# Optimization experiments

Measured on AMD Instinct MI355X. Metric: run time of the kernel, lower is better.

Reference implementation:

```python
import jax, jax.numpy as jnp
import numpy as np

B, S, D = 4, 2048, 1024
H = 16
HD = D // H
PF = 4096
EPS = 1e-5


def setup_inputs() -> dict:
    key = jax.random.key(0)
    ks = jax.random.split(key, 16)
    s = 1.0 / np.sqrt(D)
    inp = {
        'src': jax.random.normal(ks[0], (B, S, D), jnp.float32),
        'Wq': jax.random.normal(ks[1], (D, D), jnp.float32) * s,
        'bq': jnp.zeros((D,), jnp.float32),
        'Wk': jax.random.normal(ks[2], (D, D), jnp.float32) * s,
        'bk': jnp.zeros((D,), jnp.float32),
        'Wv': jax.random.normal(ks[3], (D, D), jnp.float32) * s,
        'bv': jnp.zeros((D,), jnp.float32),
        'Wo': jax.random.normal(ks[4], (D, D), jnp.float32) * s,
        'bo': jnp.zeros((D,), jnp.float32),
        'g1': jnp.ones((D,), jnp.float32),
        'b1': jnp.zeros((D,), jnp.float32),
        'W1': jax.random.normal(ks[5], (D, PF), jnp.float32) * s,
        'bf1': jnp.zeros((PF,), jnp.float32),
        'W2': jax.random.normal(ks[6], (PF, D), jnp.float32) * (1.0 / np.sqrt(PF)),
        'bf2': jnp.zeros((D,), jnp.float32),
        'g2': jnp.ones((D,), jnp.float32),
        'b2': jnp.zeros((D,), jnp.float32),
    }
    return inp


def _layer_norm(x, g, b):
    mu = jnp.mean(x, axis=-1, keepdims=True)
    var = jnp.mean(jnp.square(x - mu), axis=-1, keepdims=True)
    return (x - mu) * jax.lax.rsqrt(var + EPS) * g + b


def reference(src, Wq, bq, Wk, bk, Wv, bv, Wo, bo, g1, b1, W1, bf1, W2, bf2, g2, b2):
    scale = 1.0 / np.sqrt(HD)
    # QKV projections -> [B, H, S, HD]
    q = (src @ Wq + bq).reshape(B, S, H, HD).transpose(0, 2, 1, 3)
    k = (src @ Wk + bk).reshape(B, S, H, HD).transpose(0, 2, 1, 3)
    v = (src @ Wv + bv).reshape(B, S, H, HD).transpose(0, 2, 1, 3)
    # attention scores [B, H, S, S]
    attn = jax.nn.softmax(jnp.einsum('bhqd,bhkd->bhqk', q, k) * scale, axis=-1)
    x = jnp.einsum('bhqk,bhkd->bhqd', attn, v)
    x = x.transpose(0, 2, 1, 3).reshape(B, S, D)
    attn_out = x @ Wo + bo
    # residual + LN (dropout is identity at p=0)
    src1 = _layer_norm(src + attn_out, g1, b1)
    # positionwise FFN: Linear -> Dropout -> ReLU -> Linear
    ff = jax.nn.relu(src1 @ W1 + bf1) @ W2 + bf2
    return _layer_norm(src1 + ff, g2, b2)
```

## Files before the change

kernel.cpp:

```cpp
#include <hip/hip_runtime.h>

#define BB 4
#define SS 2048
#define DD 1024
#define HH 16
#define PFF 4096
#define MR 8192

typedef unsigned short u16;
typedef __attribute__((ext_vector_type(8))) short s16x8;
typedef __attribute__((ext_vector_type(4))) float f32x4v;
typedef __attribute__((ext_vector_type(4))) unsigned short u16x4;
typedef __attribute__((ext_vector_type(8))) unsigned short u16x8;

__device__ inline u16 f2bf(float f) {
  union { float f; unsigned u; } v; v.f = f;
  unsigned r = v.u + 0x7FFFu + ((v.u >> 16) & 1u);
  return (u16)(r >> 16);
}

__device__ inline void gload16(const void* g, void* l) {
  __builtin_amdgcn_global_load_lds(
      (const __attribute__((address_space(1))) void*)g,
      (__attribute__((address_space(3))) void*)l, 16, 0, 0);
}

__device__ inline f32x4v MFMA(s16x8 a, s16x8 b, f32x4v c) {
  return __builtin_amdgcn_mfma_f32_16x16x32_bf16(a, b, c, 0, 0, 0);
}

__device__ inline s16x8 ldfrag(const u16* base, int row, int colByte) {
  return *(const s16x8*)((const char*)base + row * 128 + (colByte ^ ((row & 7) << 4)));
}

template <int RELU, int OUTBF>
__global__ __launch_bounds__(256) void gemm_bf16(
    const u16* __restrict__ A, const u16* __restrict__ Bt,
    const float* __restrict__ bias, float* __restrict__ Cf,
    u16* __restrict__ Cb, int M, int N, int K) {
  __shared__ __align__(128) u16 As[128 * 32];
  __shared__ __align__(128) u16 Bs[128 * 32];
  const int t = threadIdx.x;
  const int lane = t & 63, w = t >> 6;
  const int wr = w >> 1, wc = w & 1;
  const int g = lane >> 4, q = lane & 15;
  const int row0 = blockIdx.y * 128, col0 = blockIdx.x * 128;

  f32x4v acc[4][4];
#pragma unroll
  for (int m = 0; m < 4; ++m)
#pragma unroll
    for (int n = 0; n < 4; ++n) acc[m][n] = (f32x4v){0.f, 0.f, 0.f, 0.f};

  const int c0 = t, c1 = 256 + t;
  const int ar0 = c0 >> 2, ac0 = (c0 & 3) * 8;
  const int ar1 = c1 >> 2, ac1 = (c1 & 3) * 8;
  const u16* Ar0 = A + (size_t)(row0 + ar0) * K + ac0;
  const u16* Ar1 = A + (size_t)(row0 + ar1) * K + ac1;
  const u16* Br0 = Bt + (size_t)(col0 + ar0) * K + ac0;
  const u16* Br1 = Bt + (size_t)(col0 + ar1) * K + ac1;
  char* AsB = (char*)As;
  char* BsB = (char*)Bs;
  const int ldst = (t & ~63) * 16;

  for (int k0 = 0; k0 < K; k0 += 32) {
    __syncthreads();
    gload16(Ar0 + k0, AsB + ldst);
    gload16(Ar1 + k0, AsB + 4096 + ldst);
    gload16(Br0 + k0, BsB + ldst);
    gload16(Br1 + k0, BsB + 4096 + ldst);
    __syncthreads();
    s16x8 af[4], bfr[4];
#pragma unroll
    for (int m = 0; m < 4; ++m)
      af[m] = *(const s16x8*)&As[(wr * 64 + 16 * m + q) * 32 + g * 8];
#pragma unroll
    for (int n = 0; n < 4; ++n)
      bfr[n] = *(const s16x8*)&Bs[(wc * 64 + 16 * n + q) * 32 + g * 8];
#pragma unroll
    for (int m = 0; m < 4; ++m)
#pragma unroll
      for (int n = 0; n < 4; ++n) acc[m][n] = MFMA(af[m], bfr[n], acc[m][n]);
  }
#pragma unroll
  for (int n = 0; n < 4; ++n) {
    const int col = col0 + wc * 64 + 16 * n + q;
    const float bv = bias[col];
#pragma unroll
    for (int m = 0; m < 4; ++m) {
#pragma unroll
      for (int r = 0; r < 4; ++r) {
        const int row = row0 + wr * 64 + 16 * m + 4 * g + r;
        float v = acc[m][n][r] + bv;
        if (RELU) v = fmaxf(v, 0.f);
        if (OUTBF) Cb[(size_t)row * N + col] = f2bf(v);
        else Cf[(size_t)row * N + col] = v;
      }
    }
  }
}

__global__ __launch_bounds__(256) void attn_mfma(
    const u16* __restrict__ qkv, const u16* __restrict__ vt,
    u16* __restrict__ xb) {
  __shared__ __align__(128) u16 Qs[64 * 64];
  __shared__ __align__(128) u16 Ks[64 * 64];
  __shared__ __align__(128) u16 Vs[64 * 64];
  __shared__ __align__(128) u16 Ps[4 * 16 * 64];

  const int t = threadIdx.x;
  const int w = t >> 6;
  const int lane = t & 63;
  const int g = lane >> 4, q = lane & 15;
  const int bh = blockIdx.y;
  const int b = bh >> 4, h = bh & 15;
  const int q0 = blockIdx.x * 64;
  const int qcol = h * 64;
  const int kcol = DD + h * 64;
  const int ldst = (t & ~63) * 16;
  const u16* Pw = Ps + w * 1024;

  {
    const int r0 = t >> 3, p0 = (t & 7) ^ (r0 & 7);
    const int c1 = 256 + t, r1 = c1 >> 3, p1 = (c1 & 7) ^ (r1 & 7);
    gload16(qkv + ((size_t)(b * SS + q0 + r0) * 3072 + qcol + p0 * 8),
            (char*)Qs + ldst);
    gload16(qkv + ((size_t)(b * SS + q0 + r1) * 3072 + qcol + p1 * 8),
            (char*)Qs + 4096 + ldst);
  }

  float m_run = -1e30f, l_run = 0.f;
  f32x4v oacc[4];
#pragma unroll
  for (int n = 0; n < 4; ++n) oacc[n] = (f32x4v){0.f, 0.f, 0.f, 0.f};
  const float scale = 0.125f;

  for (int kt = 0; kt < SS / 64; ++kt) {
    const int s0 = kt * 64;
    __syncthreads();
    {
      const int r0 = t >> 3, p0 = (t & 7) ^ (r0 & 7);
      const int c1 = 256 + t, r1 = c1 >> 3, p1 = (c1 & 7) ^ (r1 & 7);
      gload16(qkv + ((size_t)(b * SS + s0 + r0) * 3072 + kcol + p0 * 8),
              (char*)Ks + ldst);
      gload16(qkv + ((size_t)(b * SS + s0 + r1) * 3072 + kcol + p1 * 8),
              (char*)Ks + 4096 + ldst);
      gload16(vt + ((size_t)(bh * 64 + r0) * SS + s0 + p0 * 8),
              (char*)Vs + ldst);
      gload16(vt + ((size_t)(bh * 64 + r1) * SS + s0 + p1 * 8),
              (char*)Vs + 4096 + ldst);
    }
    __syncthreads();

    s16x8 bq0 = ldfrag(Qs, w * 16 + q, g * 16);
    s16x8 bq1 = ldfrag(Qs, w * 16 + q, 64 + g * 16);
    f32x4v sacc[4];
#pragma unroll
    for (int m = 0; m < 4; ++m) {
      sacc[m] = (f32x4v){0.f, 0.f, 0.f, 0.f};
      s16x8 a0 = ldfrag(Ks, 16 * m + q, g * 16);
      s16x8 a1 = ldfrag(Ks, 16 * m + q, 64 + g * 16);
      sacc[m] = MFMA(a0, bq0, sacc[m]);
      sacc[m] = MFMA(a1, bq1, sacc[m]);
    }

    float sc[16];
    float tm = -1e30f;
#pragma unroll
    for (int m = 0; m < 4; ++m)
#pragma unroll
      for (int r = 0; r < 4; ++r) {
        float sv = sacc[m][r] * scale;
        sc[m * 4 + r] = sv;
        tm = fmaxf(tm, sv);
      }
    tm = fmaxf(tm, __shfl_xor(tm, 16));
    tm = fmaxf(tm, __shfl_xor(tm, 32));
    const float m_new = fmaxf(m_run, tm);
    const float rf = __expf(m_run - m_new);
    float psum = 0.f;
#pragma unroll
    for (int m = 0; m < 4; ++m) {
      u16x4 pw;
#pragma unroll
      for (int r = 0; r < 4; ++r) {
        float p = __expf(sc[m * 4 + r] - m_new);
        psum += p;
        pw[r] = f2bf(p);
      }
      const int cb = (32 * m + 8 * g) ^ ((q & 7) << 4);
      *(u16x4*)((char*)(Ps + w * 1024) + q * 128 + cb) = pw;
    }
    psum += __shfl_xor(psum, 16);
    psum += __shfl_xor(psum, 32);
    l_run = l_run * rf + psum;
    m_run = m_new;

    float rfo[4];
#pragma unroll
    for (int r = 0; r < 4; ++r) rfo[r] = __shfl(rf, 4 * g + r);
#pragma unroll
    for (int n = 0; n < 4; ++n) {
      oacc[n][0] *= rfo[0]; oacc[n][1] *= rfo[1];
      oacc[n][2] *= rfo[2]; oacc[n][3] *= rfo[3];
    }

#pragma unroll
    for (int s = 0; s < 2; ++s) {
      s16x8 ap = ldfrag(Pw, q, s * 64 + g * 16);
#pragma unroll
      for (int n = 0; n < 4; ++n) {
        s16x8 bv = ldfrag(Vs, 16 * n + q, s * 64 + g * 16);
        oacc[n] = MFMA(ap, bv, oacc[n]);
      }
    }
  }

  const float invl = 1.f / l_run;
  float invo[4];
#pragma unroll
  for (int r = 0; r < 4; ++r) invo[r] = __shfl(invl, 4 * g + r);
#pragma unroll
  for (int n = 0; n < 4; ++n)
#pragma unroll
    for (int r = 0; r < 4; ++r) {
      const size_t row = (size_t)(b * SS + q0 + w * 16 + 4 * g + r);
      xb[row * DD + h * 64 + 16 * n + q] = f2bf(oacc[n][r] * invo[r]);
    }
}

__global__ __launch_bounds__(256) void cvt_bf16(const float* __restrict__ x,
                                                u16* __restrict__ y, int n4) {
  int i = blockIdx.x * 256 + threadIdx.x;
  if (i < n4) {
    float4 v = ((const float4*)x)[i];
    u16x4 o;
    o[0] = f2bf(v.x); o[1] = f2bf(v.y); o[2] = f2bf(v.z); o[3] = f2bf(v.w);
    ((u16x4*)y)[i] = o;
  }
}

__global__ __launch_bounds__(256) void transpose_w(const float* __restrict__ W,
                                                   u16* __restrict__ Wt,
                                                   int K, int N) {
  __shared__ float T[32][33];
  const int n0 = blockIdx.x * 32, k0 = blockIdx.y * 32;
  const int t = threadIdx.x;
  const int r = t >> 3, c = (t & 7) * 4;
  float4 v = *(const float4*)&W[(size_t)(k0 + r) * N + n0 + c];
  T[r][c] = v.x; T[r][c + 1] = v.y; T[r][c + 2] = v.z; T[r][c + 3] = v.w;
  __syncthreads();
  const int a = t >> 3, b0 = (t & 7) * 4;
  u16x4 o;
#pragma unroll
  for (int j = 0; j < 4; ++j) o[j] = f2bf(T[b0 + j][a]);
  *(u16x4*)&Wt[(size_t)(n0 + a) * K + k0 + b0] = o;
}

__global__ __launch_bounds__(256) void vtrans(const u16* __restrict__ qkv,
                                              u16* __restrict__ vt) {
  __shared__ u16 T[64 * 72];
  const int t = threadIdx.x;
  const int bh = blockIdx.y, b = bh >> 4, h = bh & 15;
  const int s0 = blockIdx.x * 64;
  const int vcol = 2048 + h * 64;
#pragma unroll
  for (int i = 0; i < 2; ++i) {
    int c = i * 256 + t;
    int sr = c >> 3, dc = (c & 7) * 8;
    *(u16x8*)&T[sr * 72 + dc] =
        *(const u16x8*)&qkv[(size_t)(b * SS + s0 + sr) * 3072 + vcol + dc];
  }
  __syncthreads();
#pragma unroll
  for (int i = 0; i < 2; ++i) {
    int c = i * 256 + t;
    int d = c >> 3, scnk = (c & 7) * 8;
    u16x8 o;
#pragma unroll
    for (int j = 0; j < 8; ++j) o[j] = T[(scnk + j) * 72 + d];
    *(u16x8*)&vt[(size_t)(bh * 64 + d) * SS + s0 + scnk] = o;
  }
}

__global__ __launch_bounds__(256) void concat3(const float* __restrict__ a,
                                               const float* __restrict__ b,
                                               const float* __restrict__ c,
                                               float* __restrict__ o) {
  int i = blockIdx.x * 256 + threadIdx.x;
  if (i < 3072)
    o[i] = i < 1024 ? a[i] : (i < 2048 ? b[i - 1024] : c[i - 2048]);
}

template <int WB>
__global__ __launch_bounds__(256) void ln_res(
    const float* __restrict__ X, const float* __restrict__ R,
    const float* __restrict__ g, const float* __restrict__ b,
    float* __restrict__ Y, u16* __restrict__ Yb) {
  const int row = blockIdx.x;
  const int t = threadIdx.x;
  const size_t off = (size_t)row * DD + t * 4;

  float4 x4 = *(const float4*)&X[off];
  float4 r4 = *(const float4*)&R[off];
  float v0 = x4.x + r4.x, v1 = x4.y + r4.y, v2 = x4.z + r4.z, v3 = x4.w + r4.w;

  float s1 = v0 + v1 + v2 + v3;
  float s2 = v0 * v0 + v1 * v1 + v2 * v2 + v3 * v3;
#pragma unroll
  for (int o = 1; o < 64; o <<= 1) {
    s1 += __shfl_xor(s1, o);
    s2 += __shfl_xor(s2, o);
  }
  __shared__ float red1[4], red2[4];
  if ((t & 63) == 0) {
    red1[t >> 6] = s1;
    red2[t >> 6] = s2;
  }
  __syncthreads();
  s1 = red1[0] + red1[1] + red1[2] + red1[3];
  s2 = red2[0] + red2[1] + red2[2] + red2[3];

  const float mu = s1 * (1.f / DD);
  const float var = s2 * (1.f / DD) - mu * mu;
  const float rs = rsqrtf(var + 1e-5f);

  float4 g4 = *(const float4*)&g[t * 4];
  float4 b4 = *(const float4*)&b[t * 4];
  float4 y;
  y.x = (v0 - mu) * rs * g4.x + b4.x;
  y.y = (v1 - mu) * rs * g4.y + b4.y;
  y.z = (v2 - mu) * rs * g4.z + b4.z;
  y.w = (v3 - mu) * rs * g4.w + b4.w;
  *(float4*)&Y[off] = y;
  if (WB) {
    u16x4 o;
    o[0] = f2bf(y.x); o[1] = f2bf(y.y); o[2] = f2bf(y.z); o[3] = f2bf(y.w);
    *(u16x4*)&Yb[off] = o;
  }
}

extern "C" void kernel_launch(void* const* d_in, const int* in_sizes, int n_in,
                              void* d_out, int out_size, void* d_ws,
                              size_t ws_size, hipStream_t stream) {
  const float* src = (const float*)d_in[0];
  const float* Wq  = (const float*)d_in[1];
  const float* bq  = (const float*)d_in[2];
  const float* Wk  = (const float*)d_in[3];
  const float* bk  = (const float*)d_in[4];
  const float* Wv  = (const float*)d_in[5];
  const float* bv  = (const float*)d_in[6];
  const float* Wo  = (const float*)d_in[7];
  const float* bo  = (const float*)d_in[8];
  const float* g1  = (const float*)d_in[9];
  const float* b1  = (const float*)d_in[10];
  const float* W1  = (const float*)d_in[11];
  const float* bf1 = (const float*)d_in[12];
  const float* W2  = (const float*)d_in[13];
  const float* bf2 = (const float*)d_in[14];
  const float* g2  = (const float*)d_in[15];
  const float* b2  = (const float*)d_in[16];

  char* W = (char*)d_ws;
  u16*   wqkvT = (u16*)  (W + 0);
  u16*   woT   = (u16*)  (W + 6291456);
  u16*   w1T   = (u16*)  (W + 8388608);
  u16*   w2T   = (u16*)  (W + 16777216);
  float* bqkv  = (float*)(W + 25165824);
  u16*   srcb  = (u16*)  (W + 25178112);
  u16*   qkv   = (u16*)  (W + 41955328);
  u16*   vt    = (u16*)  (W + 92286976);
  u16*   xb    = (u16*)  (W + 109064192);
  float* pb    = (float*)(W + 125841408);
  float* s1f   = (float*)(W + 159395840);
  u16*   s1bb  = (u16*)  (W + 109064192);
  u16*   f1b   = (u16*)  (W + 41955328);
  float* f2b   = (float*)(W + 125841408);

  dim3 blk(256);

  cvt_bf16<<<8192, blk, 0, stream>>>(src, srcb, MR * DD / 4);
  transpose_w<<<dim3(32, 32), blk, 0, stream>>>(Wq, wqkvT, DD, DD);
  transpose_w<<<dim3(32, 32), blk, 0, stream>>>(Wk, wqkvT + (size_t)1024 * 1024, DD, DD);
  transpose_w<<<dim3(32, 32), blk, 0, stream>>>(Wv, wqkvT + (size_t)2048 * 1024, DD, DD);
  transpose_w<<<dim3(32, 32), blk, 0, stream>>>(Wo, woT, DD, DD);
  transpose_w<<<dim3(128, 32), blk, 0, stream>>>(W1, w1T, DD, PFF);
  transpose_w<<<dim3(32, 128), blk, 0, stream>>>(W2, w2T, PFF, DD);
  concat3<<<12, blk, 0, stream>>>(bq, bk, bv, bqkv);

  gemm_bf16<0, 1><<<dim3(24, 64), blk, 0, stream>>>(srcb, wqkvT, bqkv, nullptr,
                                                    qkv, MR, 3072, DD);
  vtrans<<<dim3(32, 64), blk, 0, stream>>>(qkv, vt);
  attn_mfma<<<dim3(32, 64), blk, 0, stream>>>(qkv, vt, xb);
  gemm_bf16<0, 0><<<dim3(8, 64), blk, 0, stream>>>(xb, woT, bo, pb, nullptr,
                                                   MR, DD, DD);
  ln_res<1><<<MR, blk, 0, stream>>>(src, pb, g1, b1, s1f, s1bb);
  gemm_bf16<1, 1><<<dim3(32, 64), blk, 0, stream>>>(s1bb, w1T, bf1, nullptr,
                                                    f1b, MR, PFF, DD);
  gemm_bf16<0, 0><<<dim3(8, 64), blk, 0, stream>>>(f1b, w2T, bf2, f2b, nullptr,
                                                   MR, DD, PFF);
  ln_res<0><<<MR, blk, 0, stream>>>(s1f, f2b, g2, b2, (float*)d_out, nullptr);
}
```

Before: 531.3 us.

## Add 256x256 triple-buffered GEMM and double-buffer attention with lazy rescaling

Adds a new 512-thread GEMM kernel with 256x256 tiles, a three-stage async LDS pipeline, XCD-aware block remapping and raised wave priority around the MFMAs. It is used for the QKV and FFN1 projections. The attention kernel now double-buffers K/V tiles, hoists the Q fragments out of the loop and switches to exp2 with a prescaled log2e factor. It also skips the online-softmax rescale unless the running max grows by more than a threshold, and packs bf16 with a hardware convert instruction. The goal is to hide global-load latency and cut ALU work, at the cost of heavier LDS use, one block per CU, and unswizzled LDS reads in the new GEMM that may cause bank conflicts.

```diff
diff --git a/kernel.cpp b/kernel.cpp
--- a/kernel.cpp
+++ b/kernel.cpp
@@ -19,6 +19,12 @@
   return (u16)(r >> 16);
 }
 
+__device__ inline unsigned cvtpk_bf16(float lo, float hi) {
+  unsigned r;
+  asm("v_cvt_pk_bf16_f32 %0, %1, %2" : "=v"(r) : "v"(lo), "v"(hi));
+  return r;
+}
+
 __device__ inline void gload16(const void* g, void* l) {
   __builtin_amdgcn_global_load_lds(
       (const __attribute__((address_space(1))) void*)g,
@@ -29,8 +35,125 @@
   return __builtin_amdgcn_mfma_f32_16x16x32_bf16(a, b, c, 0, 0, 0);
 }
 
+#define RAWBAR()                          \
+  do {                                    \
+    asm volatile("" ::: "memory");        \
+    __builtin_amdgcn_s_barrier();         \
+    asm volatile("" ::: "memory");        \
+  } while (0)
+#define WAITVM(N) asm volatile("s_waitcnt vmcnt(" #N ")" ::: "memory")
+
 __device__ inline s16x8 ldfrag(const u16* base, int row, int colByte) {
   return *(const s16x8*)((const char*)base + row * 128 + (colByte ^ ((row & 7) << 4)));
+}
+
+template <int RELU, int OUTBF>
+__global__ __launch_bounds__(512, 1) void gemm256(
+    const u16* __restrict__ A, const u16* __restrict__ Bt,
+    const float* __restrict__ bias, float* __restrict__ Cf,
+    u16* __restrict__ Cb, int M, int N, int K, int ntx) {
+  __shared__ __align__(128) u16 lds[3 * 16384];
+  const int t = threadIdx.x;
+  const int lane = t & 63, w = t >> 6;
+  const int wr = w >> 2, wc = w & 3;
+  const int g = lane >> 4, q = lane & 15;
+
+  const int cpx = gridDim.x >> 3;
+  const int wg = (blockIdx.x & 7) * cpx + (blockIdx.x >> 3);
+  const int row0 = (wg / ntx) * 256, col0 = (wg % ntx) * 256;
+
+  f32x4v acc[8][4];
+#pragma unroll
+  for (int m = 0; m < 8; ++m)
+#pragma unroll
+    for (int n = 0; n < 4; ++n) acc[m][n] = (f32x4v){0.f, 0.f, 0.f, 0.f};
+
+  const int sr0 = t >> 2, sc0 = (t & 3) * 8;
+  const int sr1 = (t + 512) >> 2;
+  const u16* Ag0 = A + (size_t)(row0 + sr0) * K + sc0;
+  const u16* Ag1 = A + (size_t)(row0 + sr1) * K + sc0;
+  const u16* Bg0 = Bt + (size_t)(col0 + sr0) * K + sc0;
+  const u16* Bg1 = Bt + (size_t)(col0 + sr1) * K + sc0;
+  const int wud = (t & ~63) * 8;
+
+#define STAGE_A(kt, buf)                                          \
+  do {                                                            \
+    u16* ab_ = &lds[(buf) * 16384];                               \
+    gload16(Ag0 + (kt) * 32, ab_ + wud);                          \
+    gload16(Ag1 + (kt) * 32, ab_ + 4096 + wud);                   \
+  } while (0)
+#define STAGE_B(kt, buf)                                          \
+  do {                                                            \
+    u16* bb_ = &lds[(buf) * 16384 + 8192];                        \
+    gload16(Bg0 + (kt) * 32, bb_ + wud);                          \
+    gload16(Bg1 + (kt) * 32, bb_ + 4096 + wud);                   \
+  } while (0)
+
+  const int NT = K / 32;
+  STAGE_A(0, 0); STAGE_B(0, 0);
+  STAGE_A(1, 1); STAGE_B(1, 1);
+  WAITVM(4);
+  RAWBAR();
+
+  int cur = 0, nxt = 2;
+  for (int kt = 0; kt < NT; ++kt) {
+    const u16* ab = &lds[cur * 16384];
+    const u16* bb = ab + 8192;
+    const bool pf = (kt + 2 < NT);
+    if (pf) STAGE_A(kt + 2, nxt);
+    s16x8 bf_[4], af_[4];
+#pragma unroll
+    for (int n = 0; n < 4; ++n)
+      bf_[n] = *(const s16x8*)&bb[(wc * 64 + n * 16 + q) * 32 + g * 8];
+#pragma unroll
+    for (int m = 0; m < 4; ++m)
+      af_[m] = *(const s16x8*)&ab[(wr * 128 + m * 16 + q) * 32 + g * 8];
+    RAWBAR();
+    __builtin_amdgcn_s_setprio(1);
+#pragma unroll
+    for (int m = 0; m < 4; ++m)
+#pragma unroll
+      for (int n = 0; n < 4; ++n) acc[m][n] = MFMA(af_[m], bf_[n], acc[m][n]);
+    __builtin_amdgcn_s_setprio(0);
+    RAWBAR();
+    if (pf) STAGE_B(kt + 2, nxt);
+#pragma unroll
+    for (int m = 0; m < 4; ++m)
+      af_[m] = *(const s16x8*)&ab[(wr * 128 + (m + 4) * 16 + q) * 32 + g * 8];
+    RAWBAR();
+    __builtin_amdgcn_s_setprio(1);
+#pragma unroll
+    for (int m = 0; m < 4; ++m)
+#pragma unroll
+      for (int n = 0; n < 4; ++n) acc[m + 4][n] = MFMA(af_[m], bf_[n], acc[m + 4][n]);
+    __builtin_amdgcn_s_setprio(0);
+    if (kt + 1 < NT) {
+      if (pf) WAITVM(4);
+      else WAITVM(0);
+    }
+    RAWBAR();
+    cur = (cur == 2) ? 0 : cur + 1;
+    nxt = (nxt == 2) ? 0 : nxt + 1;
+  }
+#undef STAGE_A
+#undef STAGE_B
+
+#pragma unroll
+  for (int n = 0; n < 4; ++n) {
+    const int col = col0 + wc * 64 + 16 * n + q;
+    const float bv = bias[col];
+#pragma unroll
+    for (int m = 0; m < 8; ++m) {
+#pragma unroll
+      for (int r = 0; r < 4; ++r) {
+        const int row = row0 + wr * 128 + 16 * m + 4 * g + r;
+        float v = acc[m][n][r] + bv;
+        if (RELU) v = fmaxf(v, 0.f);
+        if (OUTBF) Cb[(size_t)row * N + col] = f2bf(v);
+        else Cf[(size_t)row * N + col] = v;
+      }
+    }
+  }
 }
 
 template <int RELU, int OUTBF>
@@ -104,65 +227,71 @@
     const u16* __restrict__ qkv, const u16* __restrict__ vt,
     u16* __restrict__ xb) {
   __shared__ __align__(128) u16 Qs[64 * 64];
-  __shared__ __align__(128) u16 Ks[64 * 64];
-  __shared__ __align__(128) u16 Vs[64 * 64];
-  __shared__ __align__(128) u16 Ps[4 * 16 * 64];
+  __shared__ __align__(128) u16 Ks[2][64 * 64];
+  __shared__ __align__(128) u16 Vs[2][64 * 64];
+  __shared__ __align__(128) u16 Ps[4][16 * 64];
 
   const int t = threadIdx.x;
-  const int w = t >> 6;
-  const int lane = t & 63;
+  const int w = t >> 6, lane = t & 63;
   const int g = lane >> 4, q = lane & 15;
-  const int bh = blockIdx.y;
-  const int b = bh >> 4, h = bh & 15;
+  const int bh = blockIdx.y, b = bh >> 4, h = bh & 15;
   const int q0 = blockIdx.x * 64;
-  const int qcol = h * 64;
-  const int kcol = DD + h * 64;
+  const int qcol = h * 64, kcol = DD + h * 64;
   const int ldst = (t & ~63) * 16;
-  const u16* Pw = Ps + w * 1024;
-
-  {
-    const int r0 = t >> 3, p0 = (t & 7) ^ (r0 & 7);
-    const int c1 = 256 + t, r1 = c1 >> 3, p1 = (c1 & 7) ^ (r1 & 7);
-    gload16(qkv + ((size_t)(b * SS + q0 + r0) * 3072 + qcol + p0 * 8),
-            (char*)Qs + ldst);
-    gload16(qkv + ((size_t)(b * SS + q0 + r1) * 3072 + qcol + p1 * 8),
-            (char*)Qs + 4096 + ldst);
-  }
+
+  const int r0 = t >> 3, c0e = ((t & 7) ^ (r0 & 7)) * 8;
+  const int r1 = (t + 256) >> 3, c1e = ((t & 7) ^ (r1 & 7)) * 8;
+  const u16* Ksrc0 = qkv + (size_t)(b * SS + r0) * 3072 + kcol + c0e;
+  const u16* Ksrc1 = qkv + (size_t)(b * SS + r1) * 3072 + kcol + c1e;
+  const u16* Vsrc0 = vt + (size_t)(bh * 64 + r0) * SS + c0e;
+  const u16* Vsrc1 = vt + (size_t)(bh * 64 + r1) * SS + c1e;
+
+  gload16(qkv + (size_t)(b * SS + q0 + r0) * 3072 + qcol + c0e, (char*)Qs + ldst);
+  gload16(qkv + (size_t)(b * SS + q0 + r1) * 3072 + qcol + c1e, (char*)Qs + 4096 + ldst);
+  gload16(Ksrc0, (char*)Ks[0] + ldst);
+  gload16(Ksrc1, (char*)Ks[0] + 4096 + ldst);
+  gload16(Vsrc0, (char*)Vs[0] + ldst);
+  gload16(Vsrc1, (char*)Vs[0] + 4096 + ldst);
+  WAITVM(0);
+  RAWBAR();
+
+  const s16x8 bq0 = ldfrag(Qs, w * 16 + q, g * 16);
+  const s16x8 bq1 = ldfrag(Qs, w * 16 + q, 64 + g * 16);
 
   float m_run = -1e30f, l_run = 0.f;
   f32x4v oacc[4];
 #pragma unroll
   for (int n = 0; n < 4; ++n) oacc[n] = (f32x4v){0.f, 0.f, 0.f, 0.f};
-  const float scale = 0.125f;
+  const float SCL2 = 0.18033688011112042f;
+
+  u16* Pw = Ps[w];
+  uint2* pdst[4];
+#pragma unroll
+  for (int m = 0; m < 4; ++m)
+    pdst[m] = (uint2*)((char*)Pw + q * 128 + ((32 * m + 8 * g) ^ ((q & 7) << 4)));
 
   for (int kt = 0; kt < SS / 64; ++kt) {
-    const int s0 = kt * 64;
-    __syncthreads();
-    {
-      const int r0 = t >> 3, p0 = (t & 7) ^ (r0 & 7);
-      const int c1 = 256 + t, r1 = c1 >> 3, p1 = (c1 & 7) ^ (r1 & 7);
-      gload16(qkv + ((size_t)(b * SS + s0 + r0) * 3072 + kcol + p0 * 8),
-              (char*)Ks + ldst);
-      gload16(qkv + ((size_t)(b * SS + s0 + r1) * 3072 + kcol + p1 * 8),
-              (char*)Ks + 4096 + ldst);
-      gload16(vt + ((size_t)(bh * 64 + r0) * SS + s0 + p0 * 8),
-              (char*)Vs + ldst);
-      gload16(vt + ((size_t)(bh * 64 + r1) * SS + s0 + p1 * 8),
-              (char*)Vs + 4096 + ldst);
-    }
-    __syncthreads();
-
-    s16x8 bq0 = ldfrag(Qs, w * 16 + q, g * 16);
-    s16x8 bq1 = ldfrag(Qs, w * 16 + q, 64 + g * 16);
+    const int cur = kt & 1;
+    if (kt < SS / 64 - 1) {
+      const size_t koff = (size_t)(kt + 1) * 64 * 3072;
+      const int voff = (kt + 1) * 64;
+      gload16(Ksrc0 + koff, (char*)Ks[cur ^ 1] + ldst);
+      gload16(Ksrc1 + koff, (char*)Ks[cur ^ 1] + 4096 + ldst);
+      gload16(Vsrc0 + voff, (char*)Vs[cur ^ 1] + ldst);
+      gload16(Vsrc1 + voff, (char*)Vs[cur ^ 1] + 4096 + ldst);
+    }
+
     f32x4v sacc[4];
+    __builtin_amdgcn_s_setprio(1);
 #pragma unroll
     for (int m = 0; m < 4; ++m) {
       sacc[m] = (f32x4v){0.f, 0.f, 0.f, 0.f};
-      s16x8 a0 = ldfrag(Ks, 16 * m + q, g * 16);
-      s16x8 a1 = ldfrag(Ks, 16 * m + q, 64 + g * 16);
+      s16x8 a0 = ldfrag(Ks[cur], 16 * m + q, g * 16);
+      s16x8 a1 = ldfrag(Ks[cur], 16 * m + q, 64 + g * 16);
       sacc[m] = MFMA(a0, bq0, sacc[m]);
       sacc[m] = MFMA(a1, bq1, sacc[m]);
     }
+    __builtin_amdgcn_s_setprio(0);
 
     float sc[16];
     float tm = -1e30f;
@@ -170,50 +299,57 @@
     for (int m = 0; m < 4; ++m)
 #pragma unroll
       for (int r = 0; r < 4; ++r) {
-        float sv = sacc[m][r] * scale;
+        float sv = sacc[m][r] * SCL2;
         sc[m * 4 + r] = sv;
         tm = fmaxf(tm, sv);
       }
     tm = fmaxf(tm, __shfl_xor(tm, 16));
     tm = fmaxf(tm, __shfl_xor(tm, 32));
-    const float m_new = fmaxf(m_run, tm);
-    const float rf = __expf(m_run - m_new);
+    if (!__all(tm <= m_run + 8.f)) {
+      const float m_new = fmaxf(m_run, tm);
+      const float rf = exp2f(m_run - m_new);
+      float rfo[4];
+#pragma unroll
+      for (int r = 0; r < 4; ++r) rfo[r] = __shfl(rf, 4 * g + r);
+#pragma unroll
+      for (int n = 0; n < 4; ++n) {
+        oacc[n][0] *= rfo[0]; oacc[n][1] *= rfo[1];
+        oacc[n][2] *= rfo[2]; oacc[n][3] *= rfo[3];
+      }
+      l_run *= rf;
+      m_run = m_new;
+    }
     float psum = 0.f;
 #pragma unroll
     for (int m = 0; m < 4; ++m) {
-      u16x4 pw;
-#pragma unroll
-      for (int r = 0; r < 4; ++r) {
-        float p = __expf(sc[m * 4 + r] - m_new);
-        psum += p;
-        pw[r] = f2bf(p);
-      }
-      const int cb = (32 * m + 8 * g) ^ ((q & 7) << 4);
-      *(u16x4*)((char*)(Ps + w * 1024) + q * 128 + cb) = pw;
+      float p0 = exp2f(sc[m * 4 + 0] - m_run);
+      float p1 = exp2f(sc[m * 4 + 1] - m_run);
+      float p2 = exp2f(sc[m * 4 + 2] - m_run);
+      float p3 = exp2f(sc[m * 4 + 3] - m_run);
+      psum += (p0 + p1) + (p2 + p3);
+      uint2 pw;
+      pw.x = cvtpk_bf16(p0, p1);
+      pw.y = cvtpk_bf16(p2, p3);
+      *pdst[m] = pw;
     }
     psum += __shfl_xor(psum, 16);
     psum += __shfl_xor(psum, 32);
-    l_run = l_run * rf + psum;
-    m_run = m_new;
-
-    float rfo[4];
-#pragma unroll
-    for (int r = 0; r < 4; ++r) rfo[r] = __shfl(rf, 4 * g + r);
-#pragma unroll
-    for (int n = 0; n < 4; ++n) {
-      oacc[n][0] *= rfo[0]; oacc[n][1] *= rfo[1];
-      oacc[n][2] *= rfo[2]; oacc[n][3] *= rfo[3];
-    }
-
+    l_run += psum;
+
+    __builtin_amdgcn_s_setprio(1);
 #pragma unroll
     for (int s = 0; s < 2; ++s) {
       s16x8 ap = ldfrag(Pw, q, s * 64 + g * 16);
 #pragma unroll
       for (int n = 0; n < 4; ++n) {
-        s16x8 bv = ldfrag(Vs, 16 * n + q, s * 64 + g * 16);
+        s16x8 bv = ldfrag(Vs[cur], 16 * n + q, s * 64 + g * 16);
         oacc[n] = MFMA(ap, bv, oacc[n]);
       }
     }
+    __builtin_amdgcn_s_setprio(0);
+
+    if (kt < SS / 64 - 1) WAITVM(0);
+    RAWBAR();
   }
 
   const float invl = 1.f / l_run;
@@ -388,15 +524,15 @@
   transpose_w<<<dim3(32, 128), blk, 0, stream>>>(W2, w2T, PFF, DD);
   concat3<<<12, blk, 0, stream>>>(bq, bk, bv, bqkv);
 
-  gemm_bf16<0, 1><<<dim3(24, 64), blk, 0, stream>>>(srcb, wqkvT, bqkv, nullptr,
-                                                    qkv, MR, 3072, DD);
+  gemm256<0, 1><<<384, 512, 0, stream>>>(srcb, wqkvT, bqkv, nullptr, qkv,
+                                         MR, 3072, DD, 12);
   vtrans<<<dim3(32, 64), blk, 0, stream>>>(qkv, vt);
   attn_mfma<<<dim3(32, 64), blk, 0, stream>>>(qkv, vt, xb);
   gemm_bf16<0, 0><<<dim3(8, 64), blk, 0, stream>>>(xb, woT, bo, pb, nullptr,
                                                    MR, DD, DD);
   ln_res<1><<<MR, blk, 0, stream>>>(src, pb, g1, b1, s1f, s1bb);
-  gemm_bf16<1, 1><<<dim3(32, 64), blk, 0, stream>>>(s1bb, w1T, bf1, nullptr,
-                                                    f1b, MR, PFF, DD);
+  gemm256<1, 1><<<512, 512, 0, stream>>>(s1bb, w1T, bf1, nullptr, f1b,
+                                         MR, PFF, DD, 16);
   gemm_bf16<0, 0><<<dim3(8, 64), blk, 0, stream>>>(f1b, w2T, bf2, f2b, nullptr,
                                                    MR, DD, PFF);
   ln_res<0><<<MR, blk, 0, stream>>>(s1f, f2b, g2, b2, (float*)d_out, nullptr);
```

After: 534.2 us. No clear change (+0.5%).
